# Performance work log

Measured on AMD Instinct MI355X. Metric: run time of the kernel, lower is better.

Reference implementation:

```python
import jax, jax.numpy as jnp
import numpy as np
import math

B, L, D = 4, 4096, 512
P, V = 128, 8  # n_phases, value_dim
PI = math.pi

def _lin(x, w, b):
    return x @ w + b

def _gelu(x):
    return jax.nn.gelu(x, approximate=False)  # torch default exact GELU

def setup_inputs() -> dict:
    key = jax.random.key(0)
    ks = iter(jax.random.split(key, 32))
    def rn(shape, scale=0.02):
        return (jax.random.normal(next(ks), shape, dtype=jnp.float32) * scale)
    inp = {
        'x': jax.random.normal(next(ks), (B, L, D), dtype=jnp.float32),
        'pos_phases': jax.random.normal(next(ks), (L, D), dtype=jnp.float32) * PI,
        'magnitude_scale': jnp.float32(5.0),
        'w_v': rn((D, D)), 'b_v': jnp.zeros((D,), jnp.float32),
        'w_o': rn((D, D)), 'b_o': jnp.zeros((D,), jnp.float32),
        'w_m': rn((D, D)), 'b_m': jnp.zeros((D,), jnp.float32),
        'w_q': rn((D, D)), 'b_q': jnp.zeros((D,), jnp.float32),
        'w_ke': rn((D, P)), 'b_ke': jnp.zeros((P,), jnp.float32),
        'w_ve': rn((D, V)), 'b_ve': jnp.zeros((V,), jnp.float32),
        'w_s1': rn((2 * D, D)), 'b_s1': jnp.zeros((D,), jnp.float32),
        'w_s2': rn((D, P)), 'b_s2': jnp.zeros((P,), jnp.float32),
        'w_g': rn((D, 1)), 'b_g': jnp.zeros((1,), jnp.float32),
        'w_kv': rn((V, D)), 'b_kv': jnp.zeros((D,), jnp.float32),
        'ln_g': jnp.ones((2 * D,), jnp.float32), 'ln_b': jnp.zeros((2 * D,), jnp.float32),
        'w_t1': rn((2 * D, 2 * D)), 'b_t1': jnp.zeros((2 * D,), jnp.float32),
        'w_t2': rn((2 * D, D)), 'b_t2': jnp.zeros((D,), jnp.float32),
    }
    return inp

def _forward(x, pos_phases, magnitude_scale, w_v, b_v, w_o, b_o, w_m, b_m,
             w_q, b_q, w_ke, b_ke, w_ve, b_ve, w_s1, b_s1, w_s2, b_s2,
             w_g, b_g, w_kv, b_kv, ln_g, ln_b, w_t1, b_t1, w_t2, b_t2):
    b, l, d = x.shape
    phi = pos_phases[:l]                               # [L,D]
    cos_phi, sin_phi = jnp.cos(phi), jnp.sin(phi)
    # --- positional phasor memory ---
    v1 = _lin(x, w_v, b_v)                             # [B,L,D]
    magnitude = jax.nn.sigmoid(_lin(x, w_m, b_m)) * jnp.abs(magnitude_scale)
    weighted_v1 = magnitude * v1
    mem1_cos = jnp.cumsum(weighted_v1 * cos_phi, axis=1)
    mem1_sin = jnp.cumsum(weighted_v1 * sin_phi, axis=1)
    sqrt_mag = jnp.sqrt(jnp.cumsum(magnitude, axis=1) + 1e-8)
    mem1_cos = mem1_cos / sqrt_mag
    mem1_sin = mem1_sin / sqrt_mag
    phi_query = phi + _lin(x, w_q, b_q)
    pos_ret = (mem1_cos * jnp.cos(phi_query) + mem1_sin * jnp.sin(phi_query)) / math.sqrt(d)
    pos_out = _lin(pos_ret, w_o, b_o)                  # [B,L,D]
    # --- key-value phasor memory ---
    query_phase = jnp.tanh(_lin(x, w_ke, b_ke)) * PI   # [B,L,P]
    values = _lin(x, w_ve, b_ve)                       # [B,L,V]
    store_gate = jax.nn.sigmoid(_lin(x, w_g, b_g))     # [B,L,1]
    positions = jnp.arange(1, l + 1, dtype=x.dtype)[None, :, None]
    context_avg = jnp.cumsum(x, axis=1) / positions
    sk = _lin(_gelu(_lin(jnp.concatenate([x, context_avg], axis=-1), w_s1, b_s1)), w_s2, b_s2)
    storage_phase = jnp.tanh(sk) * PI                  # [B,L,P]
    gv = values * store_gate                           # [B,L,V]
    kv_bound_cos = jnp.cos(storage_phase)[..., None] * gv[:, :, None, :]  # [B,L,P,V]
    kv_bound_sin = jnp.sin(storage_phase)[..., None] * gv[:, :, None, :]
    kv_mem_cos = jnp.cumsum(kv_bound_cos, axis=1)
    kv_mem_sin = jnp.cumsum(kv_bound_sin, axis=1)
    gate_cumsum = jnp.clip(jnp.cumsum(store_gate, axis=1), 1.0, None)     # [B,L,1]
    inv = 1.0 / jnp.sqrt(gate_cumsum)[..., None]
    kv_mem_cos = kv_mem_cos * inv
    kv_mem_sin = kv_mem_sin * inv
    kv_retrieved = (jnp.cos(query_phase)[..., None] * kv_mem_cos
                    + jnp.sin(query_phase)[..., None] * kv_mem_sin).sum(axis=2) / math.sqrt(P)
    kv_out = _lin(kv_retrieved, w_kv, b_kv)            # [B,L,D]
    # --- output projection (dropout = eval/identity) ---
    combined = jnp.concatenate([pos_out, kv_out], axis=-1)  # [B,L,2D]
    mu = combined.mean(axis=-1, keepdims=True)
    var = combined.var(axis=-1, keepdims=True)
    ln = (combined - mu) / jnp.sqrt(var + 1e-5) * ln_g + ln_b
    return x + _lin(_gelu(_lin(ln, w_t1, b_t1)), w_t2, b_t2)

def reference(x, pos_phases, magnitude_scale, w_v, b_v, w_o, b_o, w_m, b_m,
              w_q, b_q, w_ke, b_ke, w_ve, b_ve, w_s1, b_s1, w_s2, b_s2,
              w_g, b_g, w_kv, b_kv, ln_g, ln_b, w_t1, b_t1, w_t2, b_t2):
    return _forward(x, pos_phases, magnitude_scale, w_v, b_v, w_o, b_o, w_m, b_m,
                    w_q, b_q, w_ke, b_ke, w_ve, b_ve, w_s1, b_s1, w_s2, b_s2,
                    w_g, b_g, w_kv, b_kv, ln_g, ln_b, w_t1, b_t1, w_t2, b_t2)
```

## Files before the change

### kernel.cpp

```cpp
#include <hip/hip_runtime.h>
#include <math.h>

#define NTOK 16384
#define LSEQ 4096
#define BATCH 4
#define DDIM 512
#define PDIM 128
#define VDIM 8
#define PI_F 3.14159265358979323846f

#define NC2 64
#define CL2 64
#define NC3 128
#define CL3 32

typedef __attribute__((ext_vector_type(8))) short bfrag8;
typedef __attribute__((ext_vector_type(4))) float facc4;

__device__ __forceinline__ float sigmoid_(float v) { return 1.0f / (1.0f + expf(-v)); }
__device__ __forceinline__ float gelu_(float v) { return 0.5f * v * (1.0f + erff(v * 0.70710678118654752f)); }

__device__ __forceinline__ unsigned short f2bf(float f) {
    unsigned int u = __builtin_bit_cast(unsigned int, f);
    u += 0x7fffu + ((u >> 16) & 1u);
    return (unsigned short)(u >> 16);
}
__device__ __forceinline__ float bf2f(unsigned short h) {
    return __builtin_bit_cast(float, ((unsigned int)h) << 16);
}
__device__ __forceinline__ float bflo(unsigned int w) { return __builtin_bit_cast(float, w << 16); }
__device__ __forceinline__ float bfhi(unsigned int w) { return __builtin_bit_cast(float, w & 0xffff0000u); }

__device__ __forceinline__ void async16(const unsigned short* g, unsigned short* l) {
    __builtin_amdgcn_global_load_lds(
        (const __attribute__((address_space(1))) unsigned int*)g,
        (__attribute__((address_space(3))) unsigned int*)l, 16, 0, 0);
}

__global__ __launch_bounds__(256) void gemm_bf16(
    const unsigned short* __restrict__ A, int ldA,
    const unsigned short* __restrict__ Wt,
    const float* __restrict__ bias, int K,
    float* __restrict__ Cf, unsigned short* __restrict__ Cb, int ldC, int colOff,
    const float* __restrict__ res, int ldRes,
    int act)
{
    __shared__ unsigned short Asm[128 * 32];
    __shared__ unsigned short Bsm[128 * 32];
    const int tid = threadIdx.x;
    const int lane = tid & 63;
    const int wv = tid >> 6;
    const int wm = wv & 1, wn = wv >> 1;
    const int quad = lane >> 4, cc = lane & 15;
    const int row0 = blockIdx.y << 7;
    const int col0 = blockIdx.x << 7;

    facc4 acc[4][4];
#pragma unroll
    for (int i = 0; i < 4; ++i)
#pragma unroll
        for (int j = 0; j < 4; ++j) acc[i][j] = (facc4){0.f, 0.f, 0.f, 0.f};

    const int rquad = tid >> 2;
    const int kq = tid & 3;

    for (int k0 = 0; k0 < K; k0 += 32) {
        __syncthreads();
        {
            const unsigned short* ga0 = A + (size_t)(row0 + rquad) * ldA + k0 + kq * 8;
            const unsigned short* ga1 = A + (size_t)(row0 + 64 + rquad) * ldA + k0 + kq * 8;
            async16(ga0, &Asm[tid * 8]);
            async16(ga1, &Asm[(256 + tid) * 8]);
            const unsigned short* gb0 = Wt + (size_t)(col0 + rquad) * K + k0 + kq * 8;
            const unsigned short* gb1 = Wt + (size_t)(col0 + 64 + rquad) * K + k0 + kq * 8;
            async16(gb0, &Bsm[tid * 8]);
            async16(gb1, &Bsm[(256 + tid) * 8]);
        }
        __syncthreads();
        bfrag8 afr[4], bfr[4];
#pragma unroll
        for (int mt = 0; mt < 4; ++mt)
            afr[mt] = *(const bfrag8*)&Asm[(wm * 64 + mt * 16 + cc) * 32 + quad * 8];
#pragma unroll
        for (int nt = 0; nt < 4; ++nt)
            bfr[nt] = *(const bfrag8*)&Bsm[(wn * 64 + nt * 16 + cc) * 32 + quad * 8];
#pragma unroll
        for (int mt = 0; mt < 4; ++mt)
#pragma unroll
            for (int nt = 0; nt < 4; ++nt)
                acc[mt][nt] = __builtin_amdgcn_mfma_f32_16x16x32_bf16(
                    afr[mt], bfr[nt], acc[mt][nt], 0, 0, 0);
    }

#pragma unroll
    for (int nt = 0; nt < 4; ++nt) {
        int col = col0 + wn * 64 + nt * 16 + cc;
        float bvv = bias[col];
#pragma unroll
        for (int mt = 0; mt < 4; ++mt) {
            int rowb = row0 + wm * 64 + mt * 16 + quad * 4;
#pragma unroll
            for (int r = 0; r < 4; ++r) {
                float v = acc[mt][nt][r] + bvv;
                if (act == 1) v = gelu_(v);
                size_t row = (size_t)(rowb + r);
                if (res) v += res[row * ldRes + col];
                size_t idx = row * ldC + colOff + col;
                if (Cf) Cf[idx] = v;
                else    Cb[idx] = f2bf(v);
            }
        }
    }
}

__global__ __launch_bounds__(256) void k_wcvt(const float* __restrict__ W, int K, int N,
                                              unsigned short* __restrict__ Wt)
{
    __shared__ float t[32][33];
    int bx = blockIdx.x, by = blockIdx.y;
    int tid = threadIdx.x;
    int tx = tid & 31, ty = tid >> 5;
#pragma unroll
    for (int r = 0; r < 4; ++r) {
        int k = by * 32 + ty + r * 8;
        t[ty + r * 8][tx] = W[(size_t)k * N + bx * 32 + tx];
    }
    __syncthreads();
#pragma unroll
    for (int r = 0; r < 4; ++r) {
        int n = bx * 32 + ty + r * 8;
        Wt[(size_t)n * K + by * 32 + tx] = f2bf(t[tx][ty + r * 8]);
    }
}

__global__ void k_xcvt(const float* __restrict__ x, unsigned short* __restrict__ xcat)
{
    int g = blockIdx.x * 256 + threadIdx.x;
    int c = g & 511, r = g >> 9;
    xcat[(size_t)r * 1024 + c] = f2bf(x[g]);
}

__global__ void k_phi(const float* __restrict__ pp, float* __restrict__ cphi,
                      float* __restrict__ sphi, int n)
{
    int i = blockIdx.x * 256 + threadIdx.x;
    if (i < n) {
        float s, c;
        sincosf(pp[i], &s, &c);
        cphi[i] = c;
        sphi[i] = s;
    }
}

__global__ __launch_bounds__(256) void k_glin(const float* __restrict__ x,
                                              const float* __restrict__ wg,
                                              const float* __restrict__ bg,
                                              float* __restrict__ glin)
{
    int wid = threadIdx.x >> 6, lane = threadIdx.x & 63;
    int row = blockIdx.x * 4 + wid;
    const float4* xr = (const float4*)(x + (size_t)row * DDIM);
    const float4* w4 = (const float4*)wg;
    float4 a0 = xr[lane], a1 = xr[lane + 64];
    float4 w0 = w4[lane], w1 = w4[lane + 64];
    float p = a0.x * w0.x + a0.y * w0.y + a0.z * w0.z + a0.w * w0.w
            + a1.x * w1.x + a1.y * w1.y + a1.z * w1.z + a1.w * w1.w;
    for (int d = 32; d >= 1; d >>= 1) p += __shfl_down(p, d, 64);
    if (lane == 0) glin[row] = p + bg[0];
}

__global__ __launch_bounds__(256) void k_values(const float* __restrict__ x,
                                                const float* __restrict__ wve,
                                                const float* __restrict__ bve,
                                                const float* __restrict__ glin,
                                                float* __restrict__ gv)
{
    int g = blockIdx.x * 256 + threadIdx.x;
    int m = g & 7, r = g >> 3;
    const float4* xr = (const float4*)(x + (size_t)r * DDIM);
    float acc = bve[m];
    for (int kq = 0; kq < 128; ++kq) {
        float4 a = xr[kq];
        int k = kq * 4;
        acc += a.x * wve[k * 8 + m] + a.y * wve[(k + 1) * 8 + m]
             + a.z * wve[(k + 2) * 8 + m] + a.w * wve[(k + 3) * 8 + m];
    }
    gv[g] = acc * sigmoid_(glin[r]);
}

__global__ __launch_bounds__(256) void k_scan1a(
    const unsigned short* __restrict__ v1, const unsigned short* __restrict__ mlin,
    const float* __restrict__ x,
    const float* __restrict__ cphi, const float* __restrict__ sphi,
    const float* __restrict__ msp, float* __restrict__ sum2)
{
    int g = blockIdx.x * 256 + threadIdx.x;
    int d = g & 511;
    int rest = g >> 9;
    int chunk = rest & (NC2 - 1);
    int b = rest >> 6;
    float msabs = fabsf(msp[0]);
    size_t base = ((size_t)b * LSEQ + chunk * CL2) * DDIM + d;
    size_t pbase = ((size_t)chunk * CL2) * DDIM + d;
    float ac = 0.f, as = 0.f, am = 0.f, ax = 0.f;
    for (int i = 0; i < CL2; ++i) {
        float ml = bf2f(mlin[base]), vv = bf2f(v1[base]), xv = x[base];
        float cp = cphi[pbase], sp = sphi[pbase];
        float mag = msabs * sigmoid_(ml);
        float wv = mag * vv;
        ac += wv * cp; as += wv * sp; am += mag; ax += xv;
        base += DDIM; pbase += DDIM;
    }
    int col = (b * DDIM + d) * NC2 + chunk;
    sum2[0 * 131072 + col] = ac;
    sum2[1 * 131072 + col] = as;
    sum2[2 * 131072 + col] = am;
    sum2[3 * 131072 + col] = ax;
}

__global__ __launch_bounds__(256) void k_scan1b(float* __restrict__ sum2)
{
    int g = blockIdx.x * 256 + threadIdx.x;
    float* p = sum2 + (size_t)g * NC2;
    float run = 0.f;
    for (int i = 0; i < NC2; ++i) { float t = p[i]; p[i] = run; run += t; }
}

__global__ __launch_bounds__(256) void k_scan1c(
    const unsigned short* __restrict__ v1, const unsigned short* __restrict__ mlin,
    const unsigned short* __restrict__ qlin, const float* __restrict__ x,
    const float* __restrict__ cphi, const float* __restrict__ sphi,
    const float* __restrict__ msp, const float* __restrict__ sum2,
    unsigned short* __restrict__ pret, unsigned short* __restrict__ xcat)
{
    int g = blockIdx.x * 256 + threadIdx.x;
    int d = g & 511;
    int rest = g >> 9;
    int chunk = rest & (NC2 - 1);
    int b = rest >> 6;
    float msabs = fabsf(msp[0]);
    int col = (b * DDIM + d) * NC2 + chunk;
    float ac = sum2[col];
    float as = sum2[131072 + col];
    float am = sum2[2 * 131072 + col];
    float ax = sum2[3 * 131072 + col];
    size_t base = ((size_t)b * LSEQ + chunk * CL2) * DDIM + d;
    size_t pbase = ((size_t)chunk * CL2) * DDIM + d;
    int l = chunk * CL2;
    const float rsd = 0.04419417382415922f;
    for (int i = 0; i < CL2; ++i, ++l) {
        float ml = bf2f(mlin[base]), vv = bf2f(v1[base]), xv = x[base];
        float q = bf2f(qlin[base]);
        float cp = cphi[pbase], sp = sphi[pbase];
        float mag = msabs * sigmoid_(ml);
        float wv = mag * vv;
        ac += wv * cp; as += wv * sp; am += mag; ax += xv;
        float inv = rsqrtf(am + 1e-8f);
        float mc = ac * inv, msn = as * inv;
        float cq, sq;
        sincosf(q, &sq, &cq);
        float cpq = cp * cq - sp * sq;
        float spq = sp * cq + cp * sq;
        pret[base] = f2bf((mc * cpq + msn * spq) * rsd);
        size_t row = (size_t)b * LSEQ + l;
        xcat[row * 1024 + 512 + d] = f2bf(ax / (float)(l + 1));
        base += DDIM; pbase += DDIM;
    }
}

__global__ void k_phases(const float* __restrict__ sk, const unsigned short* __restrict__ ke,
                         unsigned short* __restrict__ csp, unsigned short* __restrict__ ssp,
                         unsigned short* __restrict__ cqp, unsigned short* __restrict__ sqp, int n)
{
    int g = blockIdx.x * 256 + threadIdx.x;
    if (g < n) {
        float s, c;
        float spv = tanhf(sk[g]) * PI_F;
        sincosf(spv, &s, &c);
        csp[g] = f2bf(c); ssp[g] = f2bf(s);
        float qpv = tanhf(bf2f(ke[g])) * PI_F;
        sincosf(qpv, &s, &c);
        cqp[g] = f2bf(c); sqp[g] = f2bf(s);
    }
}

__global__ __launch_bounds__(1024) void k_gatescan(const float* __restrict__ glin,
                                                   float* __restrict__ gcum)
{
    __shared__ float s[1024];
    int b = blockIdx.x, tid = threadIdx.x;
    const float* gp = glin + (size_t)b * LSEQ + tid * 4;
    float e0 = sigmoid_(gp[0]);
    float e1 = sigmoid_(gp[1]);
    float e2 = sigmoid_(gp[2]);
    float e3 = sigmoid_(gp[3]);
    float l0 = e0, l1 = l0 + e1, l2 = l1 + e2, l3 = l2 + e3;
    s[tid] = l3;
    __syncthreads();
    for (int off = 1; off < 1024; off <<= 1) {
        float t = (tid >= off) ? s[tid - off] : 0.0f;
        __syncthreads();
        s[tid] += t;
        __syncthreads();
    }
    float excl = s[tid] - l3;
    float* out = gcum + (size_t)b * LSEQ + tid * 4;
    out[0] = excl + l0; out[1] = excl + l1; out[2] = excl + l2; out[3] = excl + l3;
}

__device__ __forceinline__ size_t kv_sum_idx(int b, int p, int v) {
    return ((((size_t)b * PDIM + p) * VDIM + v) * 2) * NC3;
}

__global__ __launch_bounds__(256) void k_kv1(const unsigned short* __restrict__ csp,
                                             const unsigned short* __restrict__ ssp,
                                             const float* __restrict__ gv,
                                             float* __restrict__ sum3)
{
    int blk = blockIdx.x;
    int chunk = blk & (NC3 - 1), b = blk >> 7;
    int tid = threadIdx.x;
    int w = tid >> 6, lane = tid & 63;
    int v = 2 * w + (lane & 1);
    int pq = lane >> 1;
    float sc[4] = {0, 0, 0, 0}, ss[4] = {0, 0, 0, 0};
    const uint2* c2p = (const uint2*)csp;
    const uint2* s2p = (const uint2*)ssp;
    int t = b * LSEQ + chunk * CL3;
    for (int i = 0; i < CL3; ++i, ++t) {
        uint2 cu = c2p[(size_t)t * 32 + pq];
        uint2 su = s2p[(size_t)t * 32 + pq];
        float g = gv[(size_t)t * VDIM + v];
        sc[0] += bflo(cu.x) * g; sc[1] += bfhi(cu.x) * g;
        sc[2] += bflo(cu.y) * g; sc[3] += bfhi(cu.y) * g;
        ss[0] += bflo(su.x) * g; ss[1] += bfhi(su.x) * g;
        ss[2] += bflo(su.y) * g; ss[3] += bfhi(su.y) * g;
    }
#pragma unroll
    for (int j = 0; j < 4; ++j) {
        size_t base = kv_sum_idx(b, pq * 4 + j, v) + chunk;
        sum3[base] = sc[j];
        sum3[base + NC3] = ss[j];
    }
}

__global__ __launch_bounds__(256) void k_kv2(float* __restrict__ sum3)
{
    int g = blockIdx.x * 256 + threadIdx.x;
    float* p = sum3 + (size_t)g * NC3;
    float run = 0.f;
    for (int i = 0; i < NC3; ++i) { float t = p[i]; p[i] = run; run += t; }
}

__global__ __launch_bounds__(256) void k_kv3(const unsigned short* __restrict__ csp,
                                             const unsigned short* __restrict__ ssp,
                                             const unsigned short* __restrict__ cqp,
                                             const unsigned short* __restrict__ sqp,
                                             const float* __restrict__ gv,
                                             const float* __restrict__ gcum,
                                             const float* __restrict__ sum3,
                                             float* __restrict__ kvr)
{
    int blk = blockIdx.x;
    int chunk = blk & (NC3 - 1), b = blk >> 7;
    int tid = threadIdx.x;
    int w = tid >> 6, lane = tid & 63;
    int v = 2 * w + (lane & 1);
    int pq = lane >> 1;
    float sc[4], ss[4];
#pragma unroll
    for (int j = 0; j < 4; ++j) {
        size_t base = kv_sum_idx(b, pq * 4 + j, v) + chunk;
        sc[j] = sum3[base];
        ss[j] = sum3[base + NC3];
    }
    const uint2* c2p = (const uint2*)csp;
    const uint2* s2p = (const uint2*)ssp;
    const uint2* cq2p = (const uint2*)cqp;
    const uint2* sq2p = (const uint2*)sqp;
    const float rsp = 0.08838834764831845f;
    int t = b * LSEQ + chunk * CL3;
    for (int i = 0; i < CL3; ++i, ++t) {
        uint2 cu = c2p[(size_t)t * 32 + pq];
        uint2 su = s2p[(size_t)t * 32 + pq];
        float g = gv[(size_t)t * VDIM + v];
        sc[0] += bflo(cu.x) * g; sc[1] += bfhi(cu.x) * g;
        sc[2] += bflo(cu.y) * g; sc[3] += bfhi(cu.y) * g;
        ss[0] += bflo(su.x) * g; ss[1] += bfhi(su.x) * g;
        ss[2] += bflo(su.y) * g; ss[3] += bfhi(su.y) * g;
        uint2 qcu = cq2p[(size_t)t * 32 + pq];
        uint2 qsu = sq2p[(size_t)t * 32 + pq];
        float part = bflo(qcu.x) * sc[0] + bfhi(qcu.x) * sc[1]
                   + bflo(qcu.y) * sc[2] + bfhi(qcu.y) * sc[3]
                   + bflo(qsu.x) * ss[0] + bfhi(qsu.x) * ss[1]
                   + bflo(qsu.y) * ss[2] + bfhi(qsu.y) * ss[3];
        part += __shfl_down(part, 32, 64);
        part += __shfl_down(part, 16, 64);
        part += __shfl_down(part, 8, 64);
        part += __shfl_down(part, 4, 64);
        part += __shfl_down(part, 2, 64);
        if (lane < 2) {
            float gc = gcum[t];
            float scale = rsqrtf(fmaxf(gc, 1.0f)) * rsp;
            kvr[(size_t)t * VDIM + v] = part * scale;
        }
    }
}

__global__ __launch_bounds__(256) void k_kvout(const float* __restrict__ kvr,
                                               const float* __restrict__ wkv,
                                               const float* __restrict__ bkv,
                                               unsigned short* __restrict__ comb)
{
    int g = blockIdx.x * 256 + threadIdx.x;
    int c = g & 511, r = g >> 9;
    const float* kr = kvr + (size_t)r * VDIM;
    float acc = bkv[c];
#pragma unroll
    for (int k = 0; k < 8; ++k) acc += kr[k] * wkv[k * DDIM + c];
    comb[(size_t)r * 1024 + 512 + c] = f2bf(acc);
}

__global__ __launch_bounds__(256) void k_ln(unsigned short* __restrict__ comb,
                                            const float* __restrict__ gam,
                                            const float* __restrict__ bet)
{
    int wid = threadIdx.x >> 6, lane = threadIdx.x & 63;
    int row = blockIdx.x * 4 + wid;
    unsigned int* rp = (unsigned int*)(comb + (size_t)row * 1024);
    uint4 u0 = *(uint4*)&rp[lane * 8];
    uint4 u1 = *(uint4*)&rp[lane * 8 + 4];
    unsigned int uu[8] = {u0.x, u0.y, u0.z, u0.w, u1.x, u1.y, u1.z, u1.w};
    float v[16];
    float s = 0.f, s2 = 0.f;
#pragma unroll
    for (int j = 0; j < 8; ++j) {
        v[2 * j] = bflo(uu[j]);
        v[2 * j + 1] = bfhi(uu[j]);
        s += v[2 * j] + v[2 * j + 1];
        s2 += v[2 * j] * v[2 * j] + v[2 * j + 1] * v[2 * j + 1];
    }
    for (int m = 32; m >= 1; m >>= 1) {
        s += __shfl_xor(s, m, 64);
        s2 += __shfl_xor(s2, m, 64);
    }
    float mu = s * (1.0f / 1024.0f);
    float var = s2 * (1.0f / 1024.0f) - mu * mu;
    float inv = rsqrtf(var + 1e-5f);
    int c0 = lane * 16;
    unsigned int ou[8];
#pragma unroll
    for (int j = 0; j < 8; ++j) {
        float g0 = gam[c0 + 2 * j], g1 = gam[c0 + 2 * j + 1];
        float b0 = bet[c0 + 2 * j], b1 = bet[c0 + 2 * j + 1];
        float o0 = (v[2 * j] - mu) * inv * g0 + b0;
        float o1 = (v[2 * j + 1] - mu) * inv * g1 + b1;
        ou[j] = (unsigned int)f2bf(o0) | ((unsigned int)f2bf(o1) << 16);
    }
    *(uint4*)&rp[lane * 8] = make_uint4(ou[0], ou[1], ou[2], ou[3]);
    *(uint4*)&rp[lane * 8 + 4] = make_uint4(ou[4], ou[5], ou[6], ou[7]);
}

extern "C" void kernel_launch(void* const* d_in, const int* in_sizes, int n_in,
                              void* d_out, int out_size, void* d_ws, size_t ws_size,
                              hipStream_t stream)
{
    const float* x    = (const float*)d_in[0];
    const float* pp   = (const float*)d_in[1];
    const float* msp  = (const float*)d_in[2];
    const float* w_v  = (const float*)d_in[3];
    const float* b_v  = (const float*)d_in[4];
    const float* w_o  = (const float*)d_in[5];
    const float* b_o  = (const float*)d_in[6];
    const float* w_m  = (const float*)d_in[7];
    const float* b_m  = (const float*)d_in[8];
    const float* w_q  = (const float*)d_in[9];
    const float* b_q  = (const float*)d_in[10];
    const float* w_ke = (const float*)d_in[11];
    const float* b_ke = (const float*)d_in[12];
    const float* w_ve = (const float*)d_in[13];
    const float* b_ve = (const float*)d_in[14];
    const float* w_s1 = (const float*)d_in[15];
    const float* b_s1 = (const float*)d_in[16];
    const float* w_s2 = (const float*)d_in[17];
    const float* b_s2 = (const float*)d_in[18];
    const float* w_g  = (const float*)d_in[19];
    const float* b_g  = (const float*)d_in[20];
    const float* w_kv = (const float*)d_in[21];
    const float* b_kv = (const float*)d_in[22];
    const float* ln_g = (const float*)d_in[23];
    const float* ln_b = (const float*)d_in[24];
    const float* w_t1 = (const float*)d_in[25];
    const float* b_t1 = (const float*)d_in[26];
    const float* w_t2 = (const float*)d_in[27];
    const float* b_t2 = (const float*)d_in[28];
    float* out = (float*)d_out;
    float* ws = (float*)d_ws;
    (void)ws_size; (void)n_in; (void)in_sizes; (void)out_size;

    unsigned short* V1bf   = (unsigned short*)(ws);
    unsigned short* MLINbf = (unsigned short*)(ws + 4194304);
    float*          SKf    = ws + 4194304;
    unsigned short* QLINbf = (unsigned short*)(ws + 8388608);
    unsigned short* CSP    = (unsigned short*)(ws + 8388608);
    unsigned short* SSP    = CSP + 2097152;
    unsigned short* CQP    = CSP + 2 * 2097152;
    unsigned short* SQP    = CSP + 3 * 2097152;
    unsigned short* KEbf   = (unsigned short*)(ws + 12582912);
    float* GVb   = ws + 13631488;
    float* GLINb = ws + 13762560;
    float* GCUMb = ws + 13778944;
    float* SUM2b = ws + 13795328;
    float* SUM3b = ws + 14319616;
    float* KVRb  = ws + 15368192;
    float* CPHIb = ws + 15499264;
    float* SPHIb = ws + 17596416;
    unsigned short* HSbf   = (unsigned short*)(ws + 15499264);
    unsigned short* PRETbf = (unsigned short*)(ws + 19693568);
    unsigned short* XCAT   = (unsigned short*)(ws + 23887872);
    unsigned short* COMBbf = XCAT;
    unsigned short* HTbf   = (unsigned short*)(ws);
    unsigned short* WT     = (unsigned short*)(ws + 32276480);
    unsigned short* wv_t  = WT;
    unsigned short* wm_t  = WT + 262144;
    unsigned short* wq_t  = WT + 524288;
    unsigned short* wo_t  = WT + 786432;
    unsigned short* wke_t = WT + 1048576;
    unsigned short* ws1_t = WT + 1114112;
    unsigned short* ws2_t = WT + 1638400;
    unsigned short* wt1_t = WT + 1703936;
    unsigned short* wt2_t = WT + 2752512;

    k_phi<<<8192, 256, 0, stream>>>(pp, CPHIb, SPHIb, 2097152);
    k_xcvt<<<32768, 256, 0, stream>>>(x, XCAT);
    k_wcvt<<<dim3(16, 16), 256, 0, stream>>>(w_v, 512, 512, wv_t);
    k_wcvt<<<dim3(16, 16), 256, 0, stream>>>(w_m, 512, 512, wm_t);
    k_wcvt<<<dim3(16, 16), 256, 0, stream>>>(w_q, 512, 512, wq_t);
    k_wcvt<<<dim3(16, 16), 256, 0, stream>>>(w_o, 512, 512, wo_t);
    k_wcvt<<<dim3(4, 16), 256, 0, stream>>>(w_ke, 512, 128, wke_t);
    k_wcvt<<<dim3(16, 32), 256, 0, stream>>>(w_s1, 1024, 512, ws1_t);
    k_wcvt<<<dim3(4, 16), 256, 0, stream>>>(w_s2, 512, 128, ws2_t);
    k_wcvt<<<dim3(32, 32), 256, 0, stream>>>(w_t1, 1024, 1024, wt1_t);
    k_wcvt<<<dim3(16, 32), 256, 0, stream>>>(w_t2, 1024, 512, wt2_t);

    gemm_bf16<<<dim3(4, 128), 256, 0, stream>>>(XCAT, 1024, wv_t, b_v, 512, nullptr, V1bf, 512, 0, nullptr, 0, 0);
    gemm_bf16<<<dim3(4, 128), 256, 0, stream>>>(XCAT, 1024, wm_t, b_m, 512, nullptr, MLINbf, 512, 0, nullptr, 0, 0);
    gemm_bf16<<<dim3(4, 128), 256, 0, stream>>>(XCAT, 1024, wq_t, b_q, 512, nullptr, QLINbf, 512, 0, nullptr, 0, 0);
    gemm_bf16<<<dim3(1, 128), 256, 0, stream>>>(XCAT, 1024, wke_t, b_ke, 512, nullptr, KEbf, 128, 0, nullptr, 0, 0);
    k_glin<<<4096, 256, 0, stream>>>(x, w_g, b_g, GLINb);
    k_values<<<512, 256, 0, stream>>>(x, w_ve, b_ve, GLINb, GVb);

    k_scan1a<<<512, 256, 0, stream>>>(V1bf, MLINbf, x, CPHIb, SPHIb, msp, SUM2b);
    k_scan1b<<<32, 256, 0, stream>>>(SUM2b);
    k_scan1c<<<512, 256, 0, stream>>>(V1bf, MLINbf, QLINbf, x, CPHIb, SPHIb, msp, SUM2b, PRETbf, XCAT);

    gemm_bf16<<<dim3(4, 128), 256, 0, stream>>>(XCAT, 1024, ws1_t, b_s1, 1024, nullptr, HSbf, 512, 0, nullptr, 0, 1);
    gemm_bf16<<<dim3(1, 128), 256, 0, stream>>>(HSbf, 512, ws2_t, b_s2, 512, SKf, nullptr, 128, 0, nullptr, 0, 0);

    k_phases<<<8192, 256, 0, stream>>>(SKf, KEbf, CSP, SSP, CQP, SQP, 2097152);
    k_gatescan<<<4, 1024, 0, stream>>>(GLINb, GCUMb);

    k_kv1<<<512, 256, 0, stream>>>(CSP, SSP, GVb, SUM3b);
    k_kv2<<<32, 256, 0, stream>>>(SUM3b);
    k_kv3<<<512, 256, 0, stream>>>(CSP, SSP, CQP, SQP, GVb, GCUMb, SUM3b, KVRb);

    gemm_bf16<<<dim3(4, 128), 256, 0, stream>>>(PRETbf, 512, wo_t, b_o, 512, nullptr, COMBbf, 1024, 0, nullptr, 0, 0);
    k_kvout<<<32768, 256, 0, stream>>>(KVRb, w_kv, b_kv, COMBbf);
    k_ln<<<4096, 256, 0, stream>>>(COMBbf, ln_g, ln_b);
    gemm_bf16<<<dim3(8, 128), 256, 0, stream>>>(COMBbf, 1024, wt1_t, b_t1, 1024, nullptr, HTbf, 1024, 0, nullptr, 0, 1);
    gemm_bf16<<<dim3(4, 128), 256, 0, stream>>>(HTbf, 1024, wt2_t, b_t2, 1024, out, nullptr, 512, 0, x, 512, 0);
}
```

Measured before the change: 667.4 us.

## Fuse projection GEMMs, phase epilogues, LN+kv-out, and use fast math intrinsics

The four input projections (v, m, q, ke) are merged into one GEMM over concatenated weights, and the tanh/sin/cos phase computation moves into the GEMM epilogues, which removes the separate k_phases pass and the fp32 SK buffer. The GEMM gets XCD-aware block remapping and a k-major LDS layout. Several other changes ride along: the kv_out projection is fused into the LayerNorm kernel, the gate and value kernels are merged, cos/sin of the positional phases are stored as bf16, and fast intrinsics (__expf, __sinf, tanh-approximate GELU) are used. These cut launches and memory traffic but add accuracy risk, since the exact erf GELU becomes the tanh approximation and phases are computed with low-precision trig.

```diff
diff --git a/kernel.cpp b/kernel.cpp
--- a/kernel.cpp
+++ b/kernel.cpp
@@ -17,8 +17,16 @@
 typedef __attribute__((ext_vector_type(8))) short bfrag8;
 typedef __attribute__((ext_vector_type(4))) float facc4;
 
-__device__ __forceinline__ float sigmoid_(float v) { return 1.0f / (1.0f + expf(-v)); }
-__device__ __forceinline__ float gelu_(float v) { return 0.5f * v * (1.0f + erff(v * 0.70710678118654752f)); }
+__device__ __forceinline__ float sigmoid_(float v) { return 1.0f / (1.0f + __expf(-v)); }
+__device__ __forceinline__ float tanh_(float x) {
+    float e = __expf(-2.0f * fabsf(x));
+    float t = (1.0f - e) / (1.0f + e);
+    return copysignf(t, x);
+}
+__device__ __forceinline__ float gelu_(float v) {
+    float u = 0.7978845608028654f * (v + 0.044715f * v * v * v);
+    return 0.5f * v * (1.0f + tanh_(u));
+}
 
 __device__ __forceinline__ unsigned short f2bf(float f) {
     unsigned int u = __builtin_bit_cast(unsigned int, f);
@@ -41,49 +49,54 @@
     const unsigned short* __restrict__ A, int ldA,
     const unsigned short* __restrict__ Wt,
     const float* __restrict__ bias, int K,
-    float* __restrict__ Cf, unsigned short* __restrict__ Cb, int ldC, int colOff,
-    const float* __restrict__ res, int ldRes,
-    int act)
-{
-    __shared__ unsigned short Asm[128 * 32];
-    __shared__ unsigned short Bsm[128 * 32];
+    int nct, int nrt, int mode,
+    unsigned short* __restrict__ Ob, int ldC, int colOff,
+    float* __restrict__ Of, const float* __restrict__ res,
+    unsigned short* __restrict__ X0, unsigned short* __restrict__ X1,
+    unsigned short* __restrict__ X2, unsigned short* __restrict__ X3)
+{
+    __shared__ unsigned short Asm[4096];
+    __shared__ unsigned short Bsm[4096];
     const int tid = threadIdx.x;
     const int lane = tid & 63;
     const int wv = tid >> 6;
     const int wm = wv & 1, wn = wv >> 1;
     const int quad = lane >> 4, cc = lane & 15;
-    const int row0 = blockIdx.y << 7;
-    const int col0 = blockIdx.x << 7;
+
+    int id = blockIdx.x;
+    int xcd = id & 7;
+    int per = id >> 3;
+    int ct = per % nct;
+    int rt = xcd * (nrt >> 3) + per / nct;
+    const int row0 = rt << 7;
+    const int col0 = ct << 7;
 
     facc4 acc[4][4];
 #pragma unroll
     for (int i = 0; i < 4; ++i)
 #pragma unroll
         for (int j = 0; j < 4; ++j) acc[i][j] = (facc4){0.f, 0.f, 0.f, 0.f};
-
-    const int rquad = tid >> 2;
-    const int kq = tid & 3;
 
     for (int k0 = 0; k0 < K; k0 += 32) {
         __syncthreads();
         {
-            const unsigned short* ga0 = A + (size_t)(row0 + rquad) * ldA + k0 + kq * 8;
-            const unsigned short* ga1 = A + (size_t)(row0 + 64 + rquad) * ldA + k0 + kq * 8;
-            async16(ga0, &Asm[tid * 8]);
-            async16(ga1, &Asm[(256 + tid) * 8]);
-            const unsigned short* gb0 = Wt + (size_t)(col0 + rquad) * K + k0 + kq * 8;
-            const unsigned short* gb1 = Wt + (size_t)(col0 + 64 + rquad) * K + k0 + kq * 8;
-            async16(gb0, &Bsm[tid * 8]);
-            async16(gb1, &Bsm[(256 + tid) * 8]);
+            const unsigned short* ga0 = A + (size_t)(row0 + lane) * ldA + k0 + wv * 8;
+            const unsigned short* ga1 = A + (size_t)(row0 + 64 + lane) * ldA + k0 + wv * 8;
+            async16(ga0, &Asm[(wv * 128 + lane) * 8]);
+            async16(ga1, &Asm[(wv * 128 + 64 + lane) * 8]);
+            const unsigned short* gb0 = Wt + (size_t)(col0 + lane) * K + k0 + wv * 8;
+            const unsigned short* gb1 = Wt + (size_t)(col0 + 64 + lane) * K + k0 + wv * 8;
+            async16(gb0, &Bsm[(wv * 128 + lane) * 8]);
+            async16(gb1, &Bsm[(wv * 128 + 64 + lane) * 8]);
         }
         __syncthreads();
         bfrag8 afr[4], bfr[4];
 #pragma unroll
         for (int mt = 0; mt < 4; ++mt)
-            afr[mt] = *(const bfrag8*)&Asm[(wm * 64 + mt * 16 + cc) * 32 + quad * 8];
+            afr[mt] = *(const bfrag8*)&Asm[(quad * 128 + wm * 64 + mt * 16 + cc) * 8];
 #pragma unroll
         for (int nt = 0; nt < 4; ++nt)
-            bfr[nt] = *(const bfrag8*)&Bsm[(wn * 64 + nt * 16 + cc) * 32 + quad * 8];
+            bfr[nt] = *(const bfrag8*)&Bsm[(quad * 128 + wn * 64 + nt * 16 + cc) * 8];
 #pragma unroll
         for (int mt = 0; mt < 4; ++mt)
 #pragma unroll
@@ -102,12 +115,28 @@
 #pragma unroll
             for (int r = 0; r < 4; ++r) {
                 float v = acc[mt][nt][r] + bvv;
-                if (act == 1) v = gelu_(v);
                 size_t row = (size_t)(rowb + r);
-                if (res) v += res[row * ldRes + col];
-                size_t idx = row * ldC + colOff + col;
-                if (Cf) Cf[idx] = v;
-                else    Cb[idx] = f2bf(v);
+                if (mode == 0) {
+                    Ob[row * ldC + colOff + col] = f2bf(v);
+                } else if (mode == 1) {
+                    Ob[row * ldC + colOff + col] = f2bf(gelu_(v));
+                } else if (mode == 2) {
+                    if (col < 512)       Ob[row * 512 + col] = f2bf(v);
+                    else if (col < 1024) X0[row * 512 + col - 512] = f2bf(v);
+                    else if (col < 1536) X1[row * 512 + col - 1024] = f2bf(v);
+                    else {
+                        int c = col - 1536;
+                        float ph = tanh_(v) * PI_F;
+                        X2[row * 128 + c] = f2bf(__cosf(ph));
+                        X3[row * 128 + c] = f2bf(__sinf(ph));
+                    }
+                } else if (mode == 3) {
+                    float ph = tanh_(v) * PI_F;
+                    X2[row * 128 + col] = f2bf(__cosf(ph));
+                    X3[row * 128 + col] = f2bf(__sinf(ph));
+                } else {
+                    Of[row * 512 + col] = v + res[row * 512 + col];
+                }
             }
         }
     }
@@ -133,6 +162,16 @@
     }
 }
 
+__global__ void k_bcat(const float* __restrict__ a, const float* __restrict__ b,
+                       const float* __restrict__ c, const float* __restrict__ d,
+                       float* __restrict__ o)
+{
+    int i = blockIdx.x * 256 + threadIdx.x;
+    if (i >= 1664) return;
+    float v = (i < 512) ? a[i] : (i < 1024) ? b[i - 512] : (i < 1536) ? c[i - 1024] : d[i - 1536];
+    o[i] = v;
+}
+
 __global__ void k_xcvt(const float* __restrict__ x, unsigned short* __restrict__ xcat)
 {
     int g = blockIdx.x * 256 + threadIdx.x;
@@ -140,58 +179,62 @@
     xcat[(size_t)r * 1024 + c] = f2bf(x[g]);
 }
 
-__global__ void k_phi(const float* __restrict__ pp, float* __restrict__ cphi,
-                      float* __restrict__ sphi, int n)
+__global__ void k_phi(const float* __restrict__ pp, unsigned short* __restrict__ cphi,
+                      unsigned short* __restrict__ sphi, int n)
 {
     int i = blockIdx.x * 256 + threadIdx.x;
     if (i < n) {
-        float s, c;
-        sincosf(pp[i], &s, &c);
-        cphi[i] = c;
-        sphi[i] = s;
-    }
-}
-
-__global__ __launch_bounds__(256) void k_glin(const float* __restrict__ x,
-                                              const float* __restrict__ wg,
-                                              const float* __restrict__ bg,
-                                              float* __restrict__ glin)
+        float p = pp[i];
+        cphi[i] = f2bf(__cosf(p));
+        sphi[i] = f2bf(__sinf(p));
+    }
+}
+
+__global__ __launch_bounds__(256) void k_vg(const float* __restrict__ x,
+                                            const float* __restrict__ wve,
+                                            const float* __restrict__ bve,
+                                            const float* __restrict__ wg,
+                                            const float* __restrict__ bg,
+                                            float* __restrict__ gv,
+                                            float* __restrict__ glin)
 {
     int wid = threadIdx.x >> 6, lane = threadIdx.x & 63;
     int row = blockIdx.x * 4 + wid;
     const float4* xr = (const float4*)(x + (size_t)row * DDIM);
-    const float4* w4 = (const float4*)wg;
-    float4 a0 = xr[lane], a1 = xr[lane + 64];
-    float4 w0 = w4[lane], w1 = w4[lane + 64];
-    float p = a0.x * w0.x + a0.y * w0.y + a0.z * w0.z + a0.w * w0.w
-            + a1.x * w1.x + a1.y * w1.y + a1.z * w1.z + a1.w * w1.w;
-    for (int d = 32; d >= 1; d >>= 1) p += __shfl_down(p, d, 64);
-    if (lane == 0) glin[row] = p + bg[0];
-}
-
-__global__ __launch_bounds__(256) void k_values(const float* __restrict__ x,
-                                                const float* __restrict__ wve,
-                                                const float* __restrict__ bve,
-                                                const float* __restrict__ glin,
-                                                float* __restrict__ gv)
-{
-    int g = blockIdx.x * 256 + threadIdx.x;
-    int m = g & 7, r = g >> 3;
-    const float4* xr = (const float4*)(x + (size_t)r * DDIM);
-    float acc = bve[m];
-    for (int kq = 0; kq < 128; ++kq) {
-        float4 a = xr[kq];
-        int k = kq * 4;
-        acc += a.x * wve[k * 8 + m] + a.y * wve[(k + 1) * 8 + m]
-             + a.z * wve[(k + 2) * 8 + m] + a.w * wve[(k + 3) * 8 + m];
-    }
-    gv[g] = acc * sigmoid_(glin[r]);
+    float4 a0 = xr[lane * 2], a1 = xr[lane * 2 + 1];
+    float xs[8] = {a0.x, a0.y, a0.z, a0.w, a1.x, a1.y, a1.z, a1.w};
+    float acc[8] = {0, 0, 0, 0, 0, 0, 0, 0};
+    float accg = 0.f;
+#pragma unroll
+    for (int j = 0; j < 8; ++j) {
+        int k = lane * 8 + j;
+        const float4* wr = (const float4*)(wve + (size_t)k * 8);
+        float4 w0 = wr[0], w1 = wr[1];
+        acc[0] += xs[j] * w0.x; acc[1] += xs[j] * w0.y;
+        acc[2] += xs[j] * w0.z; acc[3] += xs[j] * w0.w;
+        acc[4] += xs[j] * w1.x; acc[5] += xs[j] * w1.y;
+        acc[6] += xs[j] * w1.z; acc[7] += xs[j] * w1.w;
+        accg += xs[j] * wg[k];
+    }
+#pragma unroll
+    for (int off = 32; off >= 1; off >>= 1) {
+#pragma unroll
+        for (int m = 0; m < 8; ++m) acc[m] += __shfl_down(acc[m], off, 64);
+        accg += __shfl_down(accg, off, 64);
+    }
+    if (lane == 0) {
+        float gl = accg + bg[0];
+        glin[row] = gl;
+        float sg = sigmoid_(gl);
+#pragma unroll
+        for (int m = 0; m < 8; ++m) gv[(size_t)row * 8 + m] = (acc[m] + bve[m]) * sg;
+    }
 }
 
 __global__ __launch_bounds__(256) void k_scan1a(
     const unsigned short* __restrict__ v1, const unsigned short* __restrict__ mlin,
     const float* __restrict__ x,
-    const float* __restrict__ cphi, const float* __restrict__ sphi,
+    const unsigned short* __restrict__ cphi, const unsigned short* __restrict__ sphi,
     const float* __restrict__ msp, float* __restrict__ sum2)
 {
     int g = blockIdx.x * 256 + threadIdx.x;
@@ -205,7 +248,7 @@
     float ac = 0.f, as = 0.f, am = 0.f, ax = 0.f;
     for (int i = 0; i < CL2; ++i) {
         float ml = bf2f(mlin[base]), vv = bf2f(v1[base]), xv = x[base];
-        float cp = cphi[pbase], sp = sphi[pbase];
+        float cp = bf2f(cphi[pbase]), sp = bf2f(sphi[pbase]);
         float mag = msabs * sigmoid_(ml);
         float wv = mag * vv;
         ac += wv * cp; as += wv * sp; am += mag; ax += xv;
@@ -229,7 +272,7 @@
 __global__ __launch_bounds__(256) void k_scan1c(
     const unsigned short* __restrict__ v1, const unsigned short* __restrict__ mlin,
     const unsigned short* __restrict__ qlin, const float* __restrict__ x,
-    const float* __restrict__ cphi, const float* __restrict__ sphi,
+    const unsigned short* __restrict__ cphi, const unsigned short* __restrict__ sphi,
     const float* __restrict__ msp, const float* __restrict__ sum2,
     unsigned short* __restrict__ pret, unsigned short* __restrict__ xcat)
 {
@@ -251,36 +294,19 @@
     for (int i = 0; i < CL2; ++i, ++l) {
         float ml = bf2f(mlin[base]), vv = bf2f(v1[base]), xv = x[base];
         float q = bf2f(qlin[base]);
-        float cp = cphi[pbase], sp = sphi[pbase];
+        float cp = bf2f(cphi[pbase]), sp = bf2f(sphi[pbase]);
         float mag = msabs * sigmoid_(ml);
         float wv = mag * vv;
         ac += wv * cp; as += wv * sp; am += mag; ax += xv;
         float inv = rsqrtf(am + 1e-8f);
         float mc = ac * inv, msn = as * inv;
-        float cq, sq;
-        sincosf(q, &sq, &cq);
+        float cq = __cosf(q), sq = __sinf(q);
         float cpq = cp * cq - sp * sq;
         float spq = sp * cq + cp * sq;
         pret[base] = f2bf((mc * cpq + msn * spq) * rsd);
         size_t row = (size_t)b * LSEQ + l;
         xcat[row * 1024 + 512 + d] = f2bf(ax / (float)(l + 1));
         base += DDIM; pbase += DDIM;
-    }
-}
-
-__global__ void k_phases(const float* __restrict__ sk, const unsigned short* __restrict__ ke,
-                         unsigned short* __restrict__ csp, unsigned short* __restrict__ ssp,
-                         unsigned short* __restrict__ cqp, unsigned short* __restrict__ sqp, int n)
-{
-    int g = blockIdx.x * 256 + threadIdx.x;
-    if (g < n) {
-        float s, c;
-        float spv = tanhf(sk[g]) * PI_F;
-        sincosf(spv, &s, &c);
-        csp[g] = f2bf(c); ssp[g] = f2bf(s);
-        float qpv = tanhf(bf2f(ke[g])) * PI_F;
-        sincosf(qpv, &s, &c);
-        cqp[g] = f2bf(c); sqp[g] = f2bf(s);
     }
 }
 
@@ -407,39 +433,46 @@
     }
 }
 
-__global__ __launch_bounds__(256) void k_kvout(const float* __restrict__ kvr,
-                                               const float* __restrict__ wkv,
-                                               const float* __restrict__ bkv,
-                                               unsigned short* __restrict__ comb)
-{
-    int g = blockIdx.x * 256 + threadIdx.x;
-    int c = g & 511, r = g >> 9;
-    const float* kr = kvr + (size_t)r * VDIM;
-    float acc = bkv[c];
-#pragma unroll
-    for (int k = 0; k < 8; ++k) acc += kr[k] * wkv[k * DDIM + c];
-    comb[(size_t)r * 1024 + 512 + c] = f2bf(acc);
-}
-
-__global__ __launch_bounds__(256) void k_ln(unsigned short* __restrict__ comb,
-                                            const float* __restrict__ gam,
-                                            const float* __restrict__ bet)
-{
-    int wid = threadIdx.x >> 6, lane = threadIdx.x & 63;
+__global__ __launch_bounds__(256) void k_lnkv(unsigned short* __restrict__ comb,
+                                              const float* __restrict__ kvr,
+                                              const float* __restrict__ wkv,
+                                              const float* __restrict__ bkv,
+                                              const float* __restrict__ gam,
+                                              const float* __restrict__ bet)
+{
+    __shared__ float wks[4096];
+    __shared__ float bks[512];
+    int tid = threadIdx.x;
+    for (int i = tid; i < 4096; i += 256) wks[i] = wkv[i];
+    for (int i = tid; i < 512; i += 256) bks[i] = bkv[i];
+    __syncthreads();
+    int wid = tid >> 6, lane = tid & 63;
     int row = blockIdx.x * 4 + wid;
-    unsigned int* rp = (unsigned int*)(comb + (size_t)row * 1024);
-    uint4 u0 = *(uint4*)&rp[lane * 8];
-    uint4 u1 = *(uint4*)&rp[lane * 8 + 4];
-    unsigned int uu[8] = {u0.x, u0.y, u0.z, u0.w, u1.x, u1.y, u1.z, u1.w};
+    unsigned short* rp = comb + (size_t)row * 1024;
     float v[16];
+    if (lane < 32) {
+        uint4 u0 = *(uint4*)(rp + lane * 16);
+        uint4 u1 = *(uint4*)(rp + lane * 16 + 8);
+        unsigned int uu[8] = {u0.x, u0.y, u0.z, u0.w, u1.x, u1.y, u1.z, u1.w};
+#pragma unroll
+        for (int j = 0; j < 8; ++j) { v[2 * j] = bflo(uu[j]); v[2 * j + 1] = bfhi(uu[j]); }
+    } else {
+        int c0 = (lane - 32) * 16;
+        const float4* kr = (const float4*)(kvr + (size_t)row * 8);
+        float4 k0 = kr[0], k1 = kr[1];
+        float kk[8] = {k0.x, k0.y, k0.z, k0.w, k1.x, k1.y, k1.z, k1.w};
+#pragma unroll
+        for (int j = 0; j < 16; ++j) {
+            int c = c0 + j;
+            float a = bks[c];
+#pragma unroll
+            for (int k = 0; k < 8; ++k) a += kk[k] * wks[k * 512 + c];
+            v[j] = a;
+        }
+    }
     float s = 0.f, s2 = 0.f;
 #pragma unroll
-    for (int j = 0; j < 8; ++j) {
-        v[2 * j] = bflo(uu[j]);
-        v[2 * j + 1] = bfhi(uu[j]);
-        s += v[2 * j] + v[2 * j + 1];
-        s2 += v[2 * j] * v[2 * j] + v[2 * j + 1] * v[2 * j + 1];
-    }
+    for (int j = 0; j < 16; ++j) { s += v[j]; s2 += v[j] * v[j]; }
     for (int m = 32; m >= 1; m >>= 1) {
         s += __shfl_xor(s, m, 64);
         s2 += __shfl_xor(s2, m, 64);
@@ -447,18 +480,18 @@
     float mu = s * (1.0f / 1024.0f);
     float var = s2 * (1.0f / 1024.0f) - mu * mu;
     float inv = rsqrtf(var + 1e-5f);
-    int c0 = lane * 16;
+    int cbase = lane * 16;
     unsigned int ou[8];
 #pragma unroll
     for (int j = 0; j < 8; ++j) {
-        float g0 = gam[c0 + 2 * j], g1 = gam[c0 + 2 * j + 1];
-        float b0 = bet[c0 + 2 * j], b1 = bet[c0 + 2 * j + 1];
+        float g0 = gam[cbase + 2 * j], g1 = gam[cbase + 2 * j + 1];
+        float b0 = bet[cbase + 2 * j], b1 = bet[cbase + 2 * j + 1];
         float o0 = (v[2 * j] - mu) * inv * g0 + b0;
         float o1 = (v[2 * j + 1] - mu) * inv * g1 + b1;
         ou[j] = (unsigned int)f2bf(o0) | ((unsigned int)f2bf(o1) << 16);
     }
-    *(uint4*)&rp[lane * 8] = make_uint4(ou[0], ou[1], ou[2], ou[3]);
-    *(uint4*)&rp[lane * 8 + 4] = make_uint4(ou[4], ou[5], ou[6], ou[7]);
+    *(uint4*)(rp + cbase) = make_uint4(ou[0], ou[1], ou[2], ou[3]);
+    *(uint4*)(rp + cbase + 8) = make_uint4(ou[4], ou[5], ou[6], ou[7]);
 }
 
 extern "C" void kernel_launch(void* const* d_in, const int* in_sizes, int n_in,
@@ -500,73 +533,74 @@
 
     unsigned short* V1bf   = (unsigned short*)(ws);
     unsigned short* MLINbf = (unsigned short*)(ws + 4194304);
-    float*          SKf    = ws + 4194304;
     unsigned short* QLINbf = (unsigned short*)(ws + 8388608);
-    unsigned short* CSP    = (unsigned short*)(ws + 8388608);
-    unsigned short* SSP    = CSP + 2097152;
-    unsigned short* CQP    = CSP + 2 * 2097152;
-    unsigned short* SQP    = CSP + 3 * 2097152;
-    unsigned short* KEbf   = (unsigned short*)(ws + 12582912);
-    float* GVb   = ws + 13631488;
-    float* GLINb = ws + 13762560;
-    float* GCUMb = ws + 13778944;
-    float* SUM2b = ws + 13795328;
-    float* SUM3b = ws + 14319616;
-    float* KVRb  = ws + 15368192;
-    float* CPHIb = ws + 15499264;
-    float* SPHIb = ws + 17596416;
-    unsigned short* HSbf   = (unsigned short*)(ws + 15499264);
-    unsigned short* PRETbf = (unsigned short*)(ws + 19693568);
-    unsigned short* XCAT   = (unsigned short*)(ws + 23887872);
+    unsigned short* CQP    = (unsigned short*)(ws + 12582912);
+    unsigned short* SQP    = (unsigned short*)(ws + 13631488);
+    unsigned short* CSP    = (unsigned short*)(ws + 14680064);
+    unsigned short* SSP    = (unsigned short*)(ws + 15728640);
+    unsigned short* HSbf   = (unsigned short*)(ws + 16777216);
+    unsigned short* PRETbf = (unsigned short*)(ws + 20971520);
+    unsigned short* CPHIbf = (unsigned short*)(ws + 25165824);
+    unsigned short* SPHIbf = (unsigned short*)(ws + 26214400);
+    float* GVb   = ws + 27262976;
+    float* GLINb = ws + 27394048;
+    float* GCUMb = ws + 27410432;
+    float* SUM2b = ws + 27426816;
+    float* SUM3b = ws + 27951104;
+    float* KVRb  = ws + 28999680;
+    unsigned short* XCAT   = (unsigned short*)(ws + 29130752);
     unsigned short* COMBbf = XCAT;
     unsigned short* HTbf   = (unsigned short*)(ws);
-    unsigned short* WT     = (unsigned short*)(ws + 32276480);
-    unsigned short* wv_t  = WT;
-    unsigned short* wm_t  = WT + 262144;
-    unsigned short* wq_t  = WT + 524288;
-    unsigned short* wo_t  = WT + 786432;
-    unsigned short* wke_t = WT + 1048576;
-    unsigned short* ws1_t = WT + 1114112;
-    unsigned short* ws2_t = WT + 1638400;
-    unsigned short* wt1_t = WT + 1703936;
-    unsigned short* wt2_t = WT + 2752512;
-
-    k_phi<<<8192, 256, 0, stream>>>(pp, CPHIb, SPHIb, 2097152);
+    unsigned short* WtF    = (unsigned short*)(ws + 37519360);
+    unsigned short* ws1_t  = (unsigned short*)(ws + 37945344);
+    unsigned short* ws2_t  = (unsigned short*)(ws + 38207488);
+    unsigned short* wo_t   = (unsigned short*)(ws + 38240256);
+    unsigned short* wt1_t  = (unsigned short*)(ws + 38371328);
+    unsigned short* wt2_t  = (unsigned short*)(ws + 38895616);
+    float* BIASF           = ws + 39157760;
+
+    k_phi<<<8192, 256, 0, stream>>>(pp, CPHIbf, SPHIbf, 2097152);
     k_xcvt<<<32768, 256, 0, stream>>>(x, XCAT);
-    k_wcvt<<<dim3(16, 16), 256, 0, stream>>>(w_v, 512, 512, wv_t);
-    k_wcvt<<<dim3(16, 16), 256, 0, stream>>>(w_m, 512, 512, wm_t);
-    k_wcvt<<<dim3(16, 16), 256, 0, stream>>>(w_q, 512, 512, wq_t);
-    k_wcvt<<<dim3(16, 16), 256, 0, stream>>>(w_o, 512, 512, wo_t);
-    k_wcvt<<<dim3(4, 16), 256, 0, stream>>>(w_ke, 512, 128, wke_t);
+    k_bcat<<<7, 256, 0, stream>>>(b_v, b_m, b_q, b_ke, BIASF);
+    k_wcvt<<<dim3(16, 16), 256, 0, stream>>>(w_v, 512, 512, WtF);
+    k_wcvt<<<dim3(16, 16), 256, 0, stream>>>(w_m, 512, 512, WtF + 512 * 512);
+    k_wcvt<<<dim3(16, 16), 256, 0, stream>>>(w_q, 512, 512, WtF + 1024 * 512);
+    k_wcvt<<<dim3(4, 16), 256, 0, stream>>>(w_ke, 512, 128, WtF + 1536 * 512);
     k_wcvt<<<dim3(16, 32), 256, 0, stream>>>(w_s1, 1024, 512, ws1_t);
     k_wcvt<<<dim3(4, 16), 256, 0, stream>>>(w_s2, 512, 128, ws2_t);
+    k_wcvt<<<dim3(16, 16), 256, 0, stream>>>(w_o, 512, 512, wo_t);
     k_wcvt<<<dim3(32, 32), 256, 0, stream>>>(w_t1, 1024, 1024, wt1_t);
     k_wcvt<<<dim3(16, 32), 256, 0, stream>>>(w_t2, 1024, 512, wt2_t);
 
-    gemm_bf16<<<dim3(4, 128), 256, 0, stream>>>(XCAT, 1024, wv_t, b_v, 512, nullptr, V1bf, 512, 0, nullptr, 0, 0);
-    gemm_bf16<<<dim3(4, 128), 256, 0, stream>>>(XCAT, 1024, wm_t, b_m, 512, nullptr, MLINbf, 512, 0, nullptr, 0, 0);
-    gemm_bf16<<<dim3(4, 128), 256, 0, stream>>>(XCAT, 1024, wq_t, b_q, 512, nullptr, QLINbf, 512, 0, nullptr, 0, 0);
-    gemm_bf16<<<dim3(1, 128), 256, 0, stream>>>(XCAT, 1024, wke_t, b_ke, 512, nullptr, KEbf, 128, 0, nullptr, 0, 0);
-    k_glin<<<4096, 256, 0, stream>>>(x, w_g, b_g, GLINb);
-    k_values<<<512, 256, 0, stream>>>(x, w_ve, b_ve, GLINb, GVb);
-
-    k_scan1a<<<512, 256, 0, stream>>>(V1bf, MLINbf, x, CPHIb, SPHIb, msp, SUM2b);
+    gemm_bf16<<<1664, 256, 0, stream>>>(XCAT, 1024, WtF, BIASF, 512, 13, 128, 2,
+                                        V1bf, 512, 0, nullptr, nullptr,
+                                        MLINbf, QLINbf, CQP, SQP);
+    k_vg<<<4096, 256, 0, stream>>>(x, w_ve, b_ve, w_g, b_g, GVb, GLINb);
+
+    k_scan1a<<<512, 256, 0, stream>>>(V1bf, MLINbf, x, CPHIbf, SPHIbf, msp, SUM2b);
     k_scan1b<<<32, 256, 0, stream>>>(SUM2b);
-    k_scan1c<<<512, 256, 0, stream>>>(V1bf, MLINbf, QLINbf, x, CPHIb, SPHIb, msp, SUM2b, PRETbf, XCAT);
-
-    gemm_bf16<<<dim3(4, 128), 256, 0, stream>>>(XCAT, 1024, ws1_t, b_s1, 1024, nullptr, HSbf, 512, 0, nullptr, 0, 1);
-    gemm_bf16<<<dim3(1, 128), 256, 0, stream>>>(HSbf, 512, ws2_t, b_s2, 512, SKf, nullptr, 128, 0, nullptr, 0, 0);
-
-    k_phases<<<8192, 256, 0, stream>>>(SKf, KEbf, CSP, SSP, CQP, SQP, 2097152);
+    k_scan1c<<<512, 256, 0, stream>>>(V1bf, MLINbf, QLINbf, x, CPHIbf, SPHIbf, msp, SUM2b, PRETbf, XCAT);
+
+    gemm_bf16<<<512, 256, 0, stream>>>(XCAT, 1024, ws1_t, b_s1, 1024, 4, 128, 1,
+                                       HSbf, 512, 0, nullptr, nullptr,
+                                       nullptr, nullptr, nullptr, nullptr);
+    gemm_bf16<<<128, 256, 0, stream>>>(HSbf, 512, ws2_t, b_s2, 512, 1, 128, 3,
+                                       nullptr, 128, 0, nullptr, nullptr,
+                                       nullptr, nullptr, CSP, SSP);
     k_gatescan<<<4, 1024, 0, stream>>>(GLINb, GCUMb);
 
     k_kv1<<<512, 256, 0, stream>>>(CSP, SSP, GVb, SUM3b);
     k_kv2<<<32, 256, 0, stream>>>(SUM3b);
     k_kv3<<<512, 256, 0, stream>>>(CSP, SSP, CQP, SQP, GVb, GCUMb, SUM3b, KVRb);
 
-    gemm_bf16<<<dim3(4, 128), 256, 0, stream>>>(PRETbf, 512, wo_t, b_o, 512, nullptr, COMBbf, 1024, 0, nullptr, 0, 0);
-    k_kvout<<<32768, 256, 0, stream>>>(KVRb, w_kv, b_kv, COMBbf);
-    k_ln<<<4096, 256, 0, stream>>>(COMBbf, ln_g, ln_b);
-    gemm_bf16<<<dim3(8, 128), 256, 0, stream>>>(COMBbf, 1024, wt1_t, b_t1, 1024, nullptr, HTbf, 1024, 0, nullptr, 0, 1);
-    gemm_bf16<<<dim3(4, 128), 256, 0, stream>>>(HTbf, 1024, wt2_t, b_t2, 1024, out, nullptr, 512, 0, x, 512, 0);
-}
+    gemm_bf16<<<512, 256, 0, stream>>>(PRETbf, 512, wo_t, b_o, 512, 4, 128, 0,
+                                       COMBbf, 1024, 0, nullptr, nullptr,
+                                       nullptr, nullptr, nullptr, nullptr);
+    k_lnkv<<<4096, 256, 0, stream>>>(COMBbf, KVRb, w_kv, b_kv, ln_g, ln_b);
+    gemm_bf16<<<1024, 256, 0, stream>>>(COMBbf, 1024, wt1_t, b_t1, 1024, 8, 128, 1,
+                                        HTbf, 1024, 0, nullptr, nullptr,
+                                        nullptr, nullptr, nullptr, nullptr);
+    gemm_bf16<<<512, 256, 0, stream>>>(HTbf, 1024, wt2_t, b_t2, 1024, 4, 128, 4,
+                                       nullptr, 512, 0, out, x,
+                                       nullptr, nullptr, nullptr, nullptr);
+}
```

Measured after the change: 783.0 us. +17.3%, slower.
